# Kernel optimization log

Hardware: AMD Instinct MI355X
Metric: run time of the kernel (lower is better)

Reference implementation:

```python
import jax, jax.numpy as jnp
import numpy as np

NUM_ROIS = 148
BSZ = 16
HID = 64
IN_CH = 128
OUT_CH = 2
N1, E1 = 131072, 2097152
N2, E2 = 2368, 37888
LRELU_SLOPE = 0.01
BN_EPS = 1e-5


def gcn_conv(x, src, dst, ew, W, b, n):
    """PyG GCNConv with edge weights and self-loops (weight 1): D^-1/2 (A+I) D^-1/2 X W + b."""
    h = x @ W  # (n, out)
    deg = jax.ops.segment_sum(ew, dst, num_segments=n) + 1.0  # self-loop weight 1
    dinv = jax.lax.rsqrt(deg)
    norm = dinv[src] * ew * dinv[dst]  # (E,)
    out = jax.ops.segment_sum(h[src] * norm[:, None], dst, num_segments=n)
    out = out + h * (dinv * dinv)[:, None]  # self-loop term: 1/deg
    return out + b


def roi_pool_mean(x, roi, batch, num_rois, bsz):
    """Segment mean keyed by (batch, roi); empty groups stay zero. Returns (bsz, num_rois*d)."""
    seg = batch * num_rois + roi
    nseg = bsz * num_rois
    sums = jax.ops.segment_sum(x, seg, num_segments=nseg)
    cnt = jax.ops.segment_sum(jnp.ones((x.shape[0],), x.dtype), seg, num_segments=nseg)
    pooled = sums / jnp.maximum(cnt, 1.0)[:, None]
    return pooled.reshape(bsz, -1)


def _params(key):
    ks = jax.random.split(key, 8)
    def lin(k, fi, fo):
        return jax.random.normal(k, (fi, fo), jnp.float32) / np.sqrt(fi)
    p = {}
    p["W1a"], p["b1a"] = lin(ks[0], IN_CH, HID), jnp.zeros((HID,), jnp.float32)
    p["W1b"], p["b1b"] = lin(ks[1], HID, HID), jnp.zeros((HID,), jnp.float32)
    p["W2a"], p["b2a"] = lin(ks[2], IN_CH, HID), jnp.zeros((HID,), jnp.float32)
    p["W2b"], p["b2b"] = lin(ks[3], HID, HID), jnp.zeros((HID,), jnp.float32)
    p["Wm1"], p["bm1"] = lin(ks[4], HID * NUM_ROIS, 1000), jnp.zeros((1000,), jnp.float32)
    p["gamma"], p["beta"] = jnp.ones((1000,), jnp.float32), jnp.zeros((1000,), jnp.float32)
    p["bn_mean"], p["bn_var"] = jnp.zeros((1000,), jnp.float32), jnp.ones((1000,), jnp.float32)
    p["Wm2"], p["bm2"] = lin(ks[5], 1000, OUT_CH), jnp.zeros((OUT_CH,), jnp.float32)
    return p


def setup_inputs() -> dict:
    key = jax.random.key(0)
    ks = jax.random.split(key, 12)
    inp = {
        "x1": jax.random.normal(ks[0], (N1, IN_CH), jnp.float32),
        "node_label": jax.random.randint(ks[1], (N1,), 0, NUM_ROIS, jnp.int32),
        "edge_index1": jax.random.randint(ks[2], (2, E1), 0, N1, jnp.int32),
        "edge_weight1": jax.random.uniform(ks[3], (E1,), jnp.float32),
        "batch1": jnp.sort(jax.random.randint(ks[4], (N1,), 0, BSZ, jnp.int32)),
        "x2": jax.random.normal(ks[5], (N2, IN_CH), jnp.float32),
        "roi_label": jax.random.randint(ks[6], (N2,), 0, NUM_ROIS, jnp.int32),
        "edge_index2": jax.random.randint(ks[7], (2, E2), 0, N2, jnp.int32),
        "edge_weight2": jax.random.uniform(ks[8], (E2,), jnp.float32),
        "batch2": jnp.sort(jax.random.randint(ks[9], (N2,), 0, BSZ, jnp.int32)),
    }
    inp.update(_params(ks[10]))
    return inp


def reference(x1, node_label, edge_index1, edge_weight1, batch1,
              x2, roi_label, edge_index2, edge_weight2, batch2,
              W1a, b1a, W1b, b1b, W2a, b2a, W2b, b2b,
              Wm1, bm1, gamma, beta, bn_mean, bn_var, Wm2, bm2):
    # ROI-graph branch (convs_roi[:-1], eval mode: dropout is identity)
    s2, d2 = edge_index2[0], edge_index2[1]
    h2 = jax.nn.relu(gcn_conv(x2, s2, d2, edge_weight2, W2a, b2a, N2))
    h2 = jax.nn.relu(gcn_conv(h2, s2, d2, edge_weight2, W2b, b2b, N2))
    embedding_roi = roi_pool_mean(h2, roi_label, batch2, NUM_ROIS, BSZ)  # (B, 148*HID)
    # fine-grained branch (convs[:-1])
    s1, d1 = edge_index1[0], edge_index1[1]
    h1 = jax.nn.relu(gcn_conv(x1, s1, d1, edge_weight1, W1a, b1a, N1))
    h1 = jax.nn.relu(gcn_conv(h1, s1, d1, edge_weight1, W1b, b1b, N1))
    embedding = roi_pool_mean(h1, node_label, batch1, NUM_ROIS, BSZ)
    # classifier on embedding + embedding_roi
    s = embedding + embedding_roi
    h = s @ Wm1 + bm1
    h = gamma * (h - bn_mean) * jax.lax.rsqrt(bn_var + BN_EPS) + beta  # BatchNorm1d (eval)
    h = jnp.where(h > 0, h, LRELU_SLOPE * h)  # LeakyReLU
    out = h @ Wm2 + bm2  # (B, OUT_CH)
    return out, embedding, embedding_roi, embedding + embedding_roi
```

## Files before the change

### kernel.cpp

```cpp
#include <hip/hip_runtime.h>
#include <hip/hip_fp16.h>

#define N1 131072
#define E1 2097152
#define N2 2368
#define E2 37888
#define NROIS 148
#define BSZ 16
#define HID 64
#define INCH 128
#define NSEG (BSZ*NROIS)
#define SDIM (NROIS*HID)
#define CLS 1000
#define OCH 2

#define KT1 148
#define KCC 64
#define CT1 4
#define SLP 20

#define NB1 512
#define BLK1 512
#define EPB (E1/BLK1)
#define NPB (N1/NB1)

#define CW1 ((N1+15)/16)
#define CW2 ((N2+15)/16)
#define PW  ((NSEG+15)/16)

#define T1 (N1/16)
#define T2 (N2/16)
#define GEMMB ((T1+T2)/4)

typedef _Float16 h8 __attribute__((ext_vector_type(8)));
typedef float f4 __attribute__((ext_vector_type(4)));

__device__ __forceinline__ unsigned packh2(float a, float b) {
    return (unsigned)__half_as_ushort(__float2half_rn(a)) |
           ((unsigned)__half_as_ushort(__float2half_rn(b)) << 16);
}

__device__ __forceinline__ void fma_lo(float& a, unsigned hb, float w) {
    asm("v_fma_mix_f32 %0, %1, %2, %0 op_sel:[0,0,0] op_sel_hi:[1,0,0]"
        : "+v"(a) : "v"(hb), "v"(w));
}
__device__ __forceinline__ void fma_hi(float& a, unsigned hb, float w) {
    asm("v_fma_mix_f32 %0, %1, %2, %0 op_sel:[1,0,0] op_sel_hi:[1,0,0]"
        : "+v"(a) : "v"(hb), "v"(w));
}


__global__ void k_hist_dst(int* __restrict__ cnt, const int* __restrict__ dst, int E) {
    int e = blockIdx.x * 256 + threadIdx.x;
    if (e < E) atomicAdd(&cnt[dst[e]], 1);
}

__global__ void k_hist_seg2(int* __restrict__ c1, const int* __restrict__ b1,
                            const int* __restrict__ l1, int n1_,
                            int* __restrict__ c2, const int* __restrict__ b2,
                            const int* __restrict__ l2, int n2_) {
    int i = blockIdx.x * 256 + threadIdx.x;
    if (i < n1_) { atomicAdd(&c1[b1[i] * NROIS + l1[i]], 1); return; }
    int j = i - n1_;
    if (j < n2_) atomicAdd(&c2[b2[j] * NROIS + l2[j]], 1);
}

__global__ void k_scan1(const int* __restrict__ in, int* __restrict__ out,
                        int* __restrict__ part, int n) {
    __shared__ int sh[256];
    int t = threadIdx.x;
    int i0 = blockIdx.x * 1024 + t * 4;
    int v0 = (i0     < n) ? in[i0]     : 0;
    int v1 = (i0 + 1 < n) ? in[i0 + 1] : 0;
    int v2 = (i0 + 2 < n) ? in[i0 + 2] : 0;
    int v3 = (i0 + 3 < n) ? in[i0 + 3] : 0;
    int tot = v0 + v1 + v2 + v3;
    sh[t] = tot; __syncthreads();
    for (int off = 1; off < 256; off <<= 1) {
        int x = 0; if (t >= off) x = sh[t - off];
        __syncthreads();
        if (t >= off) sh[t] += x;
        __syncthreads();
    }
    int excl = sh[t] - tot;
    if (t == 255) part[blockIdx.x] = sh[255];
    if (i0     < n) out[i0]     = excl;
    if (i0 + 1 < n) out[i0 + 1] = excl + v0;
    if (i0 + 2 < n) out[i0 + 2] = excl + v0 + v1;
    if (i0 + 3 < n) out[i0 + 3] = excl + v0 + v1 + v2;
}

__global__ void k_scan2(int* __restrict__ part, int cnt) {
    __shared__ int sh[256];
    int t = threadIdx.x;
    int v = (t < cnt) ? part[t] : 0;
    sh[t] = v; __syncthreads();
    for (int off = 1; off < 256; off <<= 1) {
        int x = 0; if (t >= off) x = sh[t - off];
        __syncthreads();
        if (t >= off) sh[t] += x;
        __syncthreads();
    }
    if (t < cnt) part[t] = sh[t] - v;
}

__global__ void k_scan3(int* __restrict__ out, const int* __restrict__ part, int n, int total) {
    int i = blockIdx.x * 256 + threadIdx.x;
    if (i < n) out[i] += part[i >> 10];
    if (i == 0) out[n] = total;
}

__global__ void k_scan_one(const int* __restrict__ in0, int* __restrict__ out0,
                           int* __restrict__ oo0, int n0,
                           const int* __restrict__ in1, int* __restrict__ out1,
                           int* __restrict__ oo1, int n1_) {
    __shared__ int sh[256];
    __shared__ int carry;
    const int* in; int* out; int* oo; int n;
    if (blockIdx.x == 0) { in = in0; out = out0; oo = oo0; n = n0; }
    else { if (!in1) return; in = in1; out = out1; oo = oo1; n = n1_; }
    int t = threadIdx.x;
    if (t == 0) carry = 0;
    __syncthreads();
    for (int base = 0; base < n; base += 256) {
        int i = base + t;
        int v = (i < n) ? in[i] : 0;
        sh[t] = v; __syncthreads();
        for (int off = 1; off < 256; off <<= 1) {
            int x = 0; if (t >= off) x = sh[t - off];
            __syncthreads();
            if (t >= off) sh[t] += x;
            __syncthreads();
        }
        if (i < n) {
            int e = carry + sh[t] - v;
            out[i] = e;
            if (oo) oo[i] = e;
        }
        __syncthreads();
        if (t == 255) carry += sh[255];
        __syncthreads();
    }
    if (t == 0) out[n] = carry;
}

__global__ void k_fill_edges(int2* __restrict__ edges, int* __restrict__ off,
                             const int* __restrict__ src, const int* __restrict__ dst,
                             const float* __restrict__ ew, int E) {
    int e = blockIdx.x * 256 + threadIdx.x;
    if (e >= E) return;
    int pos = atomicAdd(&off[dst[e]], 1);
    edges[pos] = make_int2(src[e], __float_as_int(ew[e]));
}

__global__ void k_fill_seg2(int* __restrict__ id1, int* __restrict__ o1,
                            const int* __restrict__ b1, const int* __restrict__ l1, int n1_,
                            int* __restrict__ id2, int* __restrict__ o2,
                            const int* __restrict__ b2, const int* __restrict__ l2, int n2_) {
    int i = blockIdx.x * 256 + threadIdx.x;
    if (i < n1_) {
        int pos = atomicAdd(&o1[b1[i] * NROIS + l1[i]], 1);
        id1[pos] = i << 7;
        return;
    }
    int j = i - n1_;
    if (j < n2_) {
        int pos = atomicAdd(&o2[b2[j] * NROIS + l2[j]], 1);
        id2[pos] = j << 7;
    }
}

__global__ void k_deg_dinv(float* __restrict__ dinv, const int* __restrict__ row,
                           const int2* __restrict__ edges, int n) {
    int d = blockIdx.x * 256 + threadIdx.x;
    if (d >= n) return;
    int a = row[d], b = row[d + 1];
    float s = 1.0f;
    for (int i = a; i < b; i++) s += __int_as_float(edges[i].y);
    dinv[d] = rsqrtf(s);
}

__global__ void k_scale(int2* __restrict__ edges, const int* __restrict__ row,
                        const float* __restrict__ dinv, int n) {
    int d = blockIdx.x * 256 + threadIdx.x;
    if (d >= n) return;
    int a = row[d], b = row[d + 1];
    float dd = dinv[d];
    for (int i = a; i < b; i++) {
        int2 e = edges[i];
        edges[i] = make_int2(e.x << 7,
                             __float_as_int(dinv[e.x] * __int_as_float(e.y) * dd));
    }
}


__global__ __launch_bounds__(256) void k_p1(int* __restrict__ bh, const int* __restrict__ dst) {
    __shared__ int cnt[NB1];
    int t = threadIdx.x, blk = blockIdx.x;
    for (int i = t; i < NB1; i += 256) cnt[i] = 0;
    __syncthreads();
    int base = blk * EPB;
    for (int i = t; i < EPB; i += 256) atomicAdd(&cnt[dst[base + i] >> 8], 1);
    __syncthreads();
    for (int b = t; b < NB1; b += 256) bh[b * BLK1 + blk] = cnt[b];
}

__global__ __launch_bounds__(256) void k_p2(int2* __restrict__ tmp, const int* __restrict__ obh,
                                            const int* __restrict__ src,
                                            const int* __restrict__ dst,
                                            const float* __restrict__ ew) {
    __shared__ int cur[NB1];
    int t = threadIdx.x, blk = blockIdx.x;
    for (int b = t; b < NB1; b += 256) cur[b] = obh[b * BLK1 + blk];
    __syncthreads();
    int base = blk * EPB;
    for (int i = t; i < EPB; i += 256) {
        int e = base + i;
        int d = dst[e];
        int pos = atomicAdd(&cur[d >> 8], 1);
        tmp[pos] = make_int2(src[e] | ((d & 255) << 17), __float_as_int(ew[e]));
    }
}

__global__ __launch_bounds__(256) void k_p3a(int* __restrict__ row1, float* __restrict__ dinv,
                                             const int2* __restrict__ tmp,
                                             const int* __restrict__ obh) {
    __shared__ int h[NPB];
    __shared__ float ws[NPB];
    __shared__ int sc[256];
    int t = threadIdx.x, b = blockIdx.x;
    h[t] = 0; ws[t] = 0.f;
    __syncthreads();
    int ebase = obh[b * BLK1];
    int eend  = (b == NB1 - 1) ? E1 : obh[(b + 1) * BLK1];
    for (int i = ebase + t; i < eend; i += 256) {
        int2 ed = tmp[i];
        int dl = (ed.x >> 17) & 255;
        atomicAdd(&h[dl], 1);
        atomicAdd(&ws[dl], __int_as_float(ed.y));
    }
    __syncthreads();
    int cnt = h[t];
    sc[t] = cnt; __syncthreads();
    for (int off = 1; off < 256; off <<= 1) {
        int x = 0; if (t >= off) x = sc[t - off];
        __syncthreads();
        if (t >= off) sc[t] += x;
        __syncthreads();
    }
    row1[b * NPB + t] = ebase + sc[t] - cnt;
    dinv[b * NPB + t] = rsqrtf(1.f + ws[t]);
    if (b == NB1 - 1 && t == 255) row1[N1] = E1;
}

__global__ __launch_bounds__(256) void k_p3b(int2* __restrict__ edges,
                                             const int2* __restrict__ tmp,
                                             const int* __restrict__ obh,
                                             const int* __restrict__ row,
                                             const float* __restrict__ dinv) {
    __shared__ int cur[NPB];
    __shared__ float dvl[NPB];
    int t = threadIdx.x, b = blockIdx.x;
    int n0 = b * NPB;
    for (int i = t; i < NPB; i += 256) {
        cur[i] = row[n0 + i];
        dvl[i] = dinv[n0 + i];
    }
    __syncthreads();
    int a  = obh[b * BLK1];
    int e_ = (b == NB1 - 1) ? E1 : obh[(b + 1) * BLK1];
    for (int i = a + t; i < e_; i += 256) {
        int2 ed = tmp[i];
        int dl = (ed.x >> 17) & 255;
        int s = ed.x & 0x1FFFF;
        int pos = atomicAdd(&cur[dl], 1);
        float w = dinv[s] * __int_as_float(ed.y) * dvl[dl];
        edges[pos] = make_int2(s << 7, __float_as_int(w));
    }
}


__device__ __forceinline__ void wfrag(uint4* __restrict__ o, const float* __restrict__ W,
                                      int KCH, int idx) {
    int lane = idx & 63;
    int rest = idx >> 6;
    int ch = rest % KCH;
    int ct = rest / KCH;
    int kr = ch * 32 + ((lane >> 4) * 8);
    int col = ct * 16 + (lane & 15);
    const float* wp = W + (size_t)kr * 64 + col;
    o[idx] = make_uint4(packh2(wp[0],   wp[64]),
                        packh2(wp[128], wp[192]),
                        packh2(wp[256], wp[320]),
                        packh2(wp[384], wp[448]));
}

__global__ void k_wprep(uint4* __restrict__ wf1a, const float* __restrict__ W1a,
                        uint4* __restrict__ wf1b, const float* __restrict__ W1b,
                        uint4* __restrict__ wf2a, const float* __restrict__ W2a,
                        uint4* __restrict__ wf2b, const float* __restrict__ W2b) {
    int idx = blockIdx.x * 256 + threadIdx.x;
    if      (idx < 1024) wfrag(wf1a, W1a, 4, idx);
    else if (idx < 1536) wfrag(wf1b, W1b, 2, idx - 1024);
    else if (idx < 2560) wfrag(wf2a, W2a, 4, idx - 1536);
    else if (idx < 3072) wfrag(wf2b, W2b, 2, idx - 2560);
}

__device__ __forceinline__ h8 loadA(const float* p) {
    float4 a = *(const float4*)p;
    float4 b = *(const float4*)(p + 4);
    union { h8 v; __half h[8]; } u;
    u.h[0] = __float2half_rn(a.x); u.h[1] = __float2half_rn(a.y);
    u.h[2] = __float2half_rn(a.z); u.h[3] = __float2half_rn(a.w);
    u.h[4] = __float2half_rn(b.x); u.h[5] = __float2half_rn(b.y);
    u.h[6] = __float2half_rn(b.z); u.h[7] = __float2half_rn(b.w);
    return u.v;
}
__device__ __forceinline__ h8 loadA(const __half* p) {
    union { h8 v; uint4 u; } u;
    u.u = *(const uint4*)p;
    return u.v;
}

template <int K, typename T>
__global__ __launch_bounds__(256) void k_gemm(__half* __restrict__ out1, const T* __restrict__ x1,
                                              const uint4* __restrict__ wfa, int t1,
                                              __half* __restrict__ out2, const T* __restrict__ x2,
                                              const uint4* __restrict__ wfb, int t2) {
    constexpr int KCH = K / 32;
    int wid = blockIdx.x * 4 + (threadIdx.x >> 6);
    int lane = threadIdx.x & 63;
    __half* out; const T* x; const uint4* wf; int row0;
    if (wid < t1) { out = out1; x = x1; wf = wfa; row0 = wid * 16; }
    else {
        int w2 = wid - t1;
        if (w2 >= t2) return;
        out = out2; x = x2; wf = wfb; row0 = w2 * 16;
    }
    int lrow = lane & 15, lg = lane >> 4;

    h8 bf[4][KCH];
#pragma unroll
    for (int ct = 0; ct < 4; ct++)
#pragma unroll
        for (int ch = 0; ch < KCH; ch++) {
            union { h8 v; uint4 u; } u;
            u.u = wf[(ct * KCH + ch) * 64 + lane];
            bf[ct][ch] = u.v;
        }

    const T* xr = x + (size_t)(row0 + lrow) * K + lg * 8;
    h8 af[KCH];
#pragma unroll
    for (int ch = 0; ch < KCH; ch++) af[ch] = loadA(xr + ch * 32);

    f4 acc[4];
#pragma unroll
    for (int ct = 0; ct < 4; ct++) acc[ct] = (f4){0.f, 0.f, 0.f, 0.f};
#pragma unroll
    for (int ch = 0; ch < KCH; ch++)
#pragma unroll
        for (int ct = 0; ct < 4; ct++)
            acc[ct] = __builtin_amdgcn_mfma_f32_16x16x32_f16(af[ch], bf[ct][ch], acc[ct], 0, 0, 0);

#pragma unroll
    for (int ct = 0; ct < 4; ct++)
#pragma unroll
        for (int r = 0; r < 4; r++)
            out[(size_t)(row0 + lg * 4 + r) * 64 + ct * 16 + lrow] = __float2half_rn(acc[ct][r]);
}

__device__ __forceinline__ void conv_wave(__half* __restrict__ out, const __half* __restrict__ h,
                                          const int2* __restrict__ edges,
                                          const int* __restrict__ row,
                                          const float* __restrict__ dinv,
                                          const float* __restrict__ bias,
                                          int d0, int n, int lane) {
    int g  = lane >> 4;
    int fl = lane & 15;
    int eh = fl >> 3;
    int f8 = fl & 7;
    int d  = d0 + g;
    bool vn = d < n;
    int a = 0, b = 0;
    if (vn) { a = row[d]; b = row[d + 1]; }
    const char* hb = (const char*)h + f8 * 16;
    float acc[8] = {0.f,0.f,0.f,0.f,0.f,0.f,0.f,0.f};

    for (int base = a; base < b; base += 16) {
        int sv = 0, wv = 0;
        if (base + fl < b) { int2 e = edges[base + fl]; sv = e.x; wv = e.y; }
        int mm = b - base; if (mm > 16) mm = 16;
        int steps = (mm + 1) >> 1;
        int idx = (g << 4) + eh;
        for (int t = 0; t < steps; t++) {
            int   s = __shfl(sv, idx + (t << 1));
            float w = __int_as_float(__shfl(wv, idx + (t << 1)));
            uint4 hv = *(const uint4*)(hb + (unsigned)s);
            fma_lo(acc[0], hv.x, w); fma_hi(acc[1], hv.x, w);
            fma_lo(acc[2], hv.y, w); fma_hi(acc[3], hv.y, w);
            fma_lo(acc[4], hv.z, w); fma_hi(acc[5], hv.z, w);
            fma_lo(acc[6], hv.w, w); fma_hi(acc[7], hv.w, w);
        }
    }
    float r[8];
#pragma unroll
    for (int f = 0; f < 8; f++) r[f] = acc[f] + __shfl_xor(acc[f], 8);
    if (vn && eh == 0) {
        float di = dinv[d];
        float sl = di * di;
        uint4 hd = *(const uint4*)(hb + ((unsigned)d << 7));
        fma_lo(r[0], hd.x, sl); fma_hi(r[1], hd.x, sl);
        fma_lo(r[2], hd.y, sl); fma_hi(r[3], hd.y, sl);
        fma_lo(r[4], hd.z, sl); fma_hi(r[5], hd.z, sl);
        fma_lo(r[6], hd.w, sl); fma_hi(r[7], hd.w, sl);
        float4 b0 = *(const float4*)(bias + f8 * 8);
        float4 b1 = *(const float4*)(bias + f8 * 8 + 4);
        uint4 ov;
        ov.x = packh2(fmaxf(r[0] + b0.x, 0.f), fmaxf(r[1] + b0.y, 0.f));
        ov.y = packh2(fmaxf(r[2] + b0.z, 0.f), fmaxf(r[3] + b0.w, 0.f));
        ov.z = packh2(fmaxf(r[4] + b1.x, 0.f), fmaxf(r[5] + b1.y, 0.f));
        ov.w = packh2(fmaxf(r[6] + b1.z, 0.f), fmaxf(r[7] + b1.w, 0.f));
        *(uint4*)(out + (size_t)d * HID + f8 * 8) = ov;
    }
}

__global__ __launch_bounds__(256) void k_conv(__half* __restrict__ o1, const __half* __restrict__ h1,
                                              const int2* __restrict__ e1, const int* __restrict__ r1,
                                              const float* __restrict__ dv1, const float* __restrict__ bi1,
                                              int n1_, int nb1_,
                                              __half* __restrict__ o2, const __half* __restrict__ h2,
                                              const int2* __restrict__ e2, const int* __restrict__ r2,
                                              const float* __restrict__ dv2, const float* __restrict__ bi2,
                                              int n2_) {
    int blk = blockIdx.x;
    int lane = threadIdx.x & 63;
    int wv = threadIdx.x >> 6;
    if (blk < nb1_) conv_wave(o1, h1, e1, r1, dv1, bi1, blk * 16 + wv * 4, n1_, lane);
    else            conv_wave(o2, h2, e2, r2, dv2, bi2, (blk - nb1_) * 16 + wv * 4, n2_, lane);
}

__device__ __forceinline__ void pool_wave(float* __restrict__ emb, const __half* __restrict__ h,
                                          const int* __restrict__ nodeid,
                                          const int* __restrict__ segrow, int s0, int lane) {
    int g  = lane >> 4;
    int fl = lane & 15;
    int eh = fl >> 3;
    int f8 = fl & 7;
    int s  = s0 + g;
    bool vs = s < NSEG;
    int a = 0, b = 0;
    if (vs) { a = segrow[s]; b = segrow[s + 1]; }
    const char* hb = (const char*)h + f8 * 16;
    float acc[8] = {0.f,0.f,0.f,0.f,0.f,0.f,0.f,0.f};

    for (int base = a; base < b; base += 16) {
        int sv = 0, wv = 0;
        if (base + fl < b) { sv = nodeid[base + fl]; wv = 0x3f800000; }
        int mm = b - base; if (mm > 16) mm = 16;
        int steps = (mm + 1) >> 1;
        int idx = (g << 4) + eh;
        for (int t = 0; t < steps; t++) {
            int   q = __shfl(sv, idx + (t << 1));
            float w = __int_as_float(__shfl(wv, idx + (t << 1)));
            uint4 hv = *(const uint4*)(hb + (unsigned)q);
            fma_lo(acc[0], hv.x, w); fma_hi(acc[1], hv.x, w);
            fma_lo(acc[2], hv.y, w); fma_hi(acc[3], hv.y, w);
            fma_lo(acc[4], hv.z, w); fma_hi(acc[5], hv.z, w);
            fma_lo(acc[6], hv.w, w); fma_hi(acc[7], hv.w, w);
        }
    }
    float r[8];
#pragma unroll
    for (int f = 0; f < 8; f++) r[f] = acc[f] + __shfl_xor(acc[f], 8);
    if (vs && eh == 0) {
        float inv = 1.0f / fmaxf((float)(b - a), 1.0f);
        float4 lo = make_float4(r[0] * inv, r[1] * inv, r[2] * inv, r[3] * inv);
        float4 hi = make_float4(r[4] * inv, r[5] * inv, r[6] * inv, r[7] * inv);
        *(float4*)(emb + (size_t)s * HID + f8 * 8)     = lo;
        *(float4*)(emb + (size_t)s * HID + f8 * 8 + 4) = hi;
    }
}

__global__ __launch_bounds__(256) void k_pool(float* __restrict__ em1, const __half* __restrict__ h1,
                                              const int* __restrict__ id1, const int* __restrict__ sr1,
                                              int nbs,
                                              float* __restrict__ em2, const __half* __restrict__ h2,
                                              const int* __restrict__ id2, const int* __restrict__ sr2) {
    int blk = blockIdx.x;
    int lane = threadIdx.x & 63;
    int wv = threadIdx.x >> 6;
    if (blk < nbs) pool_wave(em1, h1, id1, sr1, blk * 16 + wv * 4, lane);
    else           pool_wave(em2, h2, id2, sr2, (blk - nbs) * 16 + wv * 4, lane);
}


__global__ __launch_bounds__(256) void k_cls(float* __restrict__ part_,
                                             const float* __restrict__ e1,
                                             const float* __restrict__ e2,
                                             float* __restrict__ esum,
                                             const float* __restrict__ Wm1) {
    __shared__ float sl[KCC * SLP];
    int tid = threadIdx.x;
    int kt = blockIdx.x >> 2, ct = blockIdx.x & 3;
    int k0 = kt * KCC;
    bool wr = (ct == 0);
    for (int i = tid; i < KCC * 16; i += 256) {
        int kk = i & (KCC - 1), b = i >> 6;
        int idx = b * SDIM + k0 + kk;
        float v = e1[idx] + e2[idx];
        sl[kk * SLP + b] = v;
        if (wr) esum[idx] = v;
    }
    __syncthreads();
    int c = ct * 256 + tid;
    bool active = c < CLS;
    const float* wp = Wm1 + (size_t)k0 * CLS + c;
    float wv[KCC];
#pragma unroll
    for (int kk = 0; kk < KCC; kk++)
        wv[kk] = active ? wp[(size_t)kk * CLS] : 0.f;
    float acc[16];
#pragma unroll
    for (int b = 0; b < 16; b++) acc[b] = 0.f;
#pragma unroll
    for (int kk = 0; kk < KCC; kk++) {
        float w = wv[kk];
        float4 s0 = *(const float4*)(&sl[kk * SLP + 0]);
        float4 s1 = *(const float4*)(&sl[kk * SLP + 4]);
        float4 s2 = *(const float4*)(&sl[kk * SLP + 8]);
        float4 s3 = *(const float4*)(&sl[kk * SLP + 12]);
        acc[0]  += s0.x * w; acc[1]  += s0.y * w; acc[2]  += s0.z * w; acc[3]  += s0.w * w;
        acc[4]  += s1.x * w; acc[5]  += s1.y * w; acc[6]  += s1.z * w; acc[7]  += s1.w * w;
        acc[8]  += s2.x * w; acc[9]  += s2.y * w; acc[10] += s2.z * w; acc[11] += s2.w * w;
        acc[12] += s3.x * w; acc[13] += s3.y * w; acc[14] += s3.z * w; acc[15] += s3.w * w;
    }
    float* pp = part_ + (size_t)(kt * CT1 + ct) * 16 * 256;
#pragma unroll
    for (int b = 0; b < 16; b++) pp[b * 256 + tid] = acc[b];
}

__global__ void k_credbn(float* __restrict__ hact, const float* __restrict__ part_,
                         const float* __restrict__ bm1, const float* __restrict__ gamma,
                         const float* __restrict__ beta, const float* __restrict__ mean,
                         const float* __restrict__ var) {
    int idx = blockIdx.x * 256 + threadIdx.x;
    if (idx >= BSZ * CLS) return;
    int b = idx / CLS, c = idx % CLS;
    int ct = c >> 8, cl = c & 255;
    float sum = 0.f;
#pragma unroll 8
    for (int kt = 0; kt < KT1; kt++)
        sum += part_[((size_t)(kt * CT1 + ct) * 16 + b) * 256 + cl];
    float t = sum + bm1[c];
    t = gamma[c] * (t - mean[c]) * rsqrtf(var[c] + 1e-5f) + beta[c];
    hact[idx] = t > 0.f ? t : 0.01f * t;
}

__global__ void k_out(float* __restrict__ outp, const float* __restrict__ hact,
                      const float* __restrict__ Wm2, const float* __restrict__ bm2) {
    int b = blockIdx.x;
    int tid = threadIdx.x;
    int o = tid & 1, part = tid >> 1;
    float acc = (part == 0) ? bm2[o] : 0.f;
    for (int k = part; k < CLS; k += 128) acc += hact[b * CLS + k] * Wm2[k * OCH + o];
    unsafeAtomicAdd(&outp[b * OCH + o], acc);
}

extern "C" void kernel_launch(void* const* d_in, const int* in_sizes, int n_in,
                              void* d_out, int out_size, void* d_ws, size_t ws_size,
                              hipStream_t stream) {
    const float* x1  = (const float*)d_in[0];
    const int*   nl  = (const int*)d_in[1];
    const int*   ei1 = (const int*)d_in[2];
    const float* ew1 = (const float*)d_in[3];
    const int*   ba1 = (const int*)d_in[4];
    const float* x2  = (const float*)d_in[5];
    const int*   rl  = (const int*)d_in[6];
    const int*   ei2 = (const int*)d_in[7];
    const float* ew2 = (const float*)d_in[8];
    const int*   ba2 = (const int*)d_in[9];
    const float* W1a = (const float*)d_in[10];
    const float* b1a = (const float*)d_in[11];
    const float* W1b = (const float*)d_in[12];
    const float* b1b = (const float*)d_in[13];
    const float* W2a = (const float*)d_in[14];
    const float* b2a = (const float*)d_in[15];
    const float* W2b = (const float*)d_in[16];
    const float* b2b = (const float*)d_in[17];
    const float* Wm1 = (const float*)d_in[18];
    const float* bm1 = (const float*)d_in[19];
    const float* gam = (const float*)d_in[20];
    const float* bet = (const float*)d_in[21];
    const float* bmn = (const float*)d_in[22];
    const float* bvr = (const float*)d_in[23];
    const float* Wm2 = (const float*)d_in[24];
    const float* bm2 = (const float*)d_in[25];

    float* out  = (float*)d_out;
    float* emb1 = out + 32;
    float* emb2 = emb1 + NSEG * HID;
    float* esum = emb2 + NSEG * HID;

    char* p = (char*)d_ws;
    auto carve = [&](size_t nbytes) { char* q = p; p += (nbytes + 255) & ~(size_t)255; return (void*)q; };
    int*    row1    = (int*)   carve((N1 + 1) * 4);
    int2*   edges1  = (int2*)  carve((size_t)E1 * 8);
    float*  dinv1   = (float*) carve(N1 * 4);
    __half* A1h     = (__half*)carve((size_t)N1 * HID * 2);
    __half* B1h     = (__half*)carve((size_t)N1 * HID * 2);
    int*    nodeid1 = (int*)   carve(N1 * 4);
    int*    segrow1 = (int*)   carve((NSEG + 1) * 4);
    int*    segoff  = (int*)   carve(2 * NSEG * 4);
    int*    bh      = (int*)   carve((NB1 * BLK1 + 1) * 4);
    int*    obh     = (int*)   carve((NB1 * BLK1 + 1) * 4);
    int*    row2    = (int*)   carve((N2 + 1) * 4);
    int*    off2    = (int*)   carve(N2 * 4);
    int2*   edges2  = (int2*)  carve((size_t)E2 * 8);
    float*  dinv2   = (float*) carve(N2 * 4);
    __half* A2h     = (__half*)carve((size_t)N2 * HID * 2);
    __half* B2h     = (__half*)carve((size_t)N2 * HID * 2);
    int*    nodeid2 = (int*)   carve(N2 * 4);
    int*    segrow2 = (int*)   carve((NSEG + 1) * 4);
    int*    part    = (int*)   carve(256 * 4);
    float*  hact    = (float*) carve(BSZ * CLS * 4);
    uint4*  wf1a    = (uint4*) carve(1024 * 16);
    uint4*  wf1b    = (uint4*) carve(512 * 16);
    uint4*  wf2a    = (uint4*) carve(1024 * 16);
    uint4*  wf2b    = (uint4*) carve(512 * 16);
    int*    segoff1 = segoff;
    int*    segoff2 = segoff + NSEG;
    int2*  tmp1 = (int2*)B1h;
    float* clsp = (float*)B1h;

    const int* src1 = ei1;
    const int* dst1 = ei1 + E1;
    const int* src2 = ei2;
    const int* dst2 = ei2 + E2;

    hipMemsetAsync(d_out, 0, (size_t)out_size * sizeof(float), stream);

    k_wprep<<<12, 256, 0, stream>>>(wf1a, W1a, wf1b, W1b, wf2a, W2a, wf2b, W2b);

    hipMemsetAsync(off2, 0, N2 * 4, stream);
    k_hist_dst<<<(E2 + 255) / 256, 256, 0, stream>>>(off2, dst2, E2);
    k_scan_one<<<1, 256, 0, stream>>>(off2, row2, off2, N2, nullptr, nullptr, nullptr, 0);
    k_fill_edges<<<(E2 + 255) / 256, 256, 0, stream>>>(edges2, off2, src2, dst2, ew2, E2);
    k_deg_dinv<<<(N2 + 255) / 256, 256, 0, stream>>>(dinv2, row2, edges2, N2);
    k_scale<<<(N2 + 255) / 256, 256, 0, stream>>>(edges2, row2, dinv2, N2);

    k_p1<<<BLK1, 256, 0, stream>>>(bh, dst1);
    k_scan1<<<(NB1 * BLK1 + 1023) / 1024, 256, 0, stream>>>(bh, obh, part, NB1 * BLK1);
    k_scan2<<<1, 256, 0, stream>>>(part, (NB1 * BLK1 + 1023) / 1024);
    k_scan3<<<(NB1 * BLK1 + 255) / 256, 256, 0, stream>>>(obh, part, NB1 * BLK1, E1);
    k_p2<<<BLK1, 256, 0, stream>>>(tmp1, obh, src1, dst1, ew1);
    k_p3a<<<NB1, 256, 0, stream>>>(row1, dinv1, tmp1, obh);
    k_p3b<<<NB1, 256, 0, stream>>>(edges1, tmp1, obh, row1, dinv1);

    k_gemm<INCH, float><<<GEMMB, 256, 0, stream>>>(A1h, x1, wf1a, T1, A2h, x2, wf2a, T2);
    k_conv<<<CW1 + CW2, 256, 0, stream>>>(B1h, A1h, edges1, row1, dinv1, b1a, N1, CW1,
                                          B2h, A2h, edges2, row2, dinv2, b2a, N2);
    k_gemm<HID, __half><<<GEMMB, 256, 0, stream>>>(A1h, B1h, wf1b, T1, A2h, B2h, wf2b, T2);
    k_conv<<<CW1 + CW2, 256, 0, stream>>>(B1h, A1h, edges1, row1, dinv1, b1b, N1, CW1,
                                          B2h, A2h, edges2, row2, dinv2, b2b, N2);

    hipMemsetAsync(segoff, 0, 2 * NSEG * 4, stream);
    k_hist_seg2<<<(N1 + N2 + 255) / 256, 256, 0, stream>>>(segoff1, ba1, nl, N1,
                                                           segoff2, ba2, rl, N2);
    k_scan_one<<<2, 256, 0, stream>>>(segoff1, segrow1, segoff1, NSEG,
                                      segoff2, segrow2, segoff2, NSEG);
    k_fill_seg2<<<(N1 + N2 + 255) / 256, 256, 0, stream>>>(nodeid1, segoff1, ba1, nl, N1,
                                                           nodeid2, segoff2, ba2, rl, N2);
    k_pool<<<PW + PW, 256, 0, stream>>>(emb1, B1h, nodeid1, segrow1, PW,
                                        emb2, B2h, nodeid2, segrow2);

    k_cls<<<KT1 * CT1, 256, 0, stream>>>(clsp, emb1, emb2, esum, Wm1);
    k_credbn<<<(BSZ * CLS + 255) / 256, 256, 0, stream>>>(hact, clsp, bm1, gam, bet, bmn, bvr);
    k_out<<<BSZ, 256, 0, stream>>>(out, hact, Wm2, bm2);
}
```

Before: 528.2 us.

## Restructure CSR build: fold degree sum into histogram, stage bucket scatter in LDS

```diff
diff --git a/kernel.cpp b/kernel.cpp
--- a/kernel.cpp
+++ b/kernel.cpp
@@ -23,6 +23,7 @@
 #define BLK1 512
 #define EPB (E1/BLK1)
 #define NPB (N1/NB1)
+#define P3CAP 5120
 
 #define CW1 ((N1+15)/16)
 #define CW2 ((N2+15)/16)
@@ -194,88 +195,131 @@
 }
 
 
-__global__ __launch_bounds__(256) void k_p1(int* __restrict__ bh, const int* __restrict__ dst) {
+__global__ __launch_bounds__(256) void k_p1(int* __restrict__ bh, const int* __restrict__ dst,
+                                            const float* __restrict__ ew, float* __restrict__ ws) {
     __shared__ int cnt[NB1];
     int t = threadIdx.x, blk = blockIdx.x;
-    for (int i = t; i < NB1; i += 256) cnt[i] = 0;
+    cnt[t] = 0; cnt[t + 256] = 0;
     __syncthreads();
     int base = blk * EPB;
-    for (int i = t; i < EPB; i += 256) atomicAdd(&cnt[dst[base + i] >> 8], 1);
-    __syncthreads();
-    for (int b = t; b < NB1; b += 256) bh[b * BLK1 + blk] = cnt[b];
+    const int4* d4 = (const int4*)(dst + base);
+    const float4* w4 = (const float4*)(ew + base);
+    for (int i = t; i < EPB / 4; i += 256) {
+        int4 d = d4[i];
+        float4 w = w4[i];
+        atomicAdd(&cnt[d.x >> 8], 1); unsafeAtomicAdd(&ws[d.x], w.x);
+        atomicAdd(&cnt[d.y >> 8], 1); unsafeAtomicAdd(&ws[d.y], w.y);
+        atomicAdd(&cnt[d.z >> 8], 1); unsafeAtomicAdd(&ws[d.z], w.z);
+        atomicAdd(&cnt[d.w >> 8], 1); unsafeAtomicAdd(&ws[d.w], w.w);
+    }
+    __syncthreads();
+    bh[t * BLK1 + blk] = cnt[t];
+    bh[(t + 256) * BLK1 + blk] = cnt[t + 256];
+}
+
+__global__ void k_dinv(float* __restrict__ dinv, int n) {
+    int i = blockIdx.x * 256 + threadIdx.x;
+    if (i < n) dinv[i] = rsqrtf(1.f + dinv[i]);
 }
 
 __global__ __launch_bounds__(256) void k_p2(int2* __restrict__ tmp, const int* __restrict__ obh,
                                             const int* __restrict__ src,
                                             const int* __restrict__ dst,
-                                            const float* __restrict__ ew) {
+                                            const float* __restrict__ ew,
+                                            const float* __restrict__ dinv) {
+    __shared__ int2 stage[EPB];
+    __shared__ unsigned short bkt[EPB];
+    __shared__ int cnt[NB1];
+    __shared__ int lofs[NB1];
+    __shared__ int gdel[NB1];
     __shared__ int cur[NB1];
+    __shared__ int sc[256];
+    __shared__ int cbr;
     int t = threadIdx.x, blk = blockIdx.x;
-    for (int b = t; b < NB1; b += 256) cur[b] = obh[b * BLK1 + blk];
+    cnt[t] = 0; cnt[t + 256] = 0;
     __syncthreads();
     int base = blk * EPB;
+    const int4* d4 = (const int4*)(dst + base);
+    for (int i = t; i < EPB / 4; i += 256) {
+        int4 d = d4[i];
+        atomicAdd(&cnt[d.x >> 8], 1);
+        atomicAdd(&cnt[d.y >> 8], 1);
+        atomicAdd(&cnt[d.z >> 8], 1);
+        atomicAdd(&cnt[d.w >> 8], 1);
+    }
+    __syncthreads();
+    for (int r = 0; r < 2; r++) {
+        int v = cnt[r * 256 + t];
+        sc[t] = v; __syncthreads();
+        for (int off = 1; off < 256; off <<= 1) {
+            int x = 0; if (t >= off) x = sc[t - off];
+            __syncthreads();
+            if (t >= off) sc[t] += x;
+            __syncthreads();
+        }
+        lofs[r * 256 + t] = (r ? cbr : 0) + sc[t] - v;
+        if (t == 255 && r == 0) cbr = sc[255];
+        __syncthreads();
+    }
+    for (int b = t; b < NB1; b += 256) {
+        int lo = lofs[b];
+        cur[b] = lo;
+        gdel[b] = obh[b * BLK1 + blk] - lo;
+    }
+    __syncthreads();
     for (int i = t; i < EPB; i += 256) {
         int e = base + i;
         int d = dst[e];
-        int pos = atomicAdd(&cur[d >> 8], 1);
-        tmp[pos] = make_int2(src[e] | ((d & 255) << 17), __float_as_int(ew[e]));
-    }
-}
-
-__global__ __launch_bounds__(256) void k_p3a(int* __restrict__ row1, float* __restrict__ dinv,
-                                             const int2* __restrict__ tmp,
-                                             const int* __restrict__ obh) {
+        int s = src[e];
+        float w = dinv[s] * ew[e] * dinv[d];
+        int b = d >> 8;
+        int p = atomicAdd(&cur[b], 1);
+        stage[p] = make_int2(s | ((d & 255) << 17), __float_as_int(w));
+        bkt[p] = (unsigned short)b;
+    }
+    __syncthreads();
+    for (int i = t; i < EPB; i += 256)
+        tmp[gdel[bkt[i]] + i] = stage[i];
+}
+
+__global__ __launch_bounds__(256) void k_p3(int2* __restrict__ edges, int* __restrict__ row1,
+                                            const int2* __restrict__ tmp,
+                                            const int* __restrict__ obh) {
+    __shared__ int2 stage[P3CAP];
     __shared__ int h[NPB];
-    __shared__ float ws[NPB];
     __shared__ int sc[256];
+    __shared__ int cur[NPB];
     int t = threadIdx.x, b = blockIdx.x;
-    h[t] = 0; ws[t] = 0.f;
-    __syncthreads();
-    int ebase = obh[b * BLK1];
-    int eend  = (b == NB1 - 1) ? E1 : obh[(b + 1) * BLK1];
-    for (int i = ebase + t; i < eend; i += 256) {
-        int2 ed = tmp[i];
-        int dl = (ed.x >> 17) & 255;
-        atomicAdd(&h[dl], 1);
-        atomicAdd(&ws[dl], __int_as_float(ed.y));
-    }
-    __syncthreads();
-    int cnt = h[t];
-    sc[t] = cnt; __syncthreads();
+    h[t] = 0;
+    __syncthreads();
+    int A = obh[b * BLK1];
+    int Eend = (b == NB1 - 1) ? E1 : obh[(b + 1) * BLK1];
+    int len = Eend - A;
+    for (int j = t; j < len; j += 256) {
+        int2 ed = tmp[A + j];
+        if (j < P3CAP) stage[j] = ed;
+        atomicAdd(&h[(ed.x >> 17) & 255], 1);
+    }
+    __syncthreads();
+    int cnt_ = h[t];
+    sc[t] = cnt_; __syncthreads();
     for (int off = 1; off < 256; off <<= 1) {
         int x = 0; if (t >= off) x = sc[t - off];
         __syncthreads();
         if (t >= off) sc[t] += x;
         __syncthreads();
     }
-    row1[b * NPB + t] = ebase + sc[t] - cnt;
-    dinv[b * NPB + t] = rsqrtf(1.f + ws[t]);
+    int excl = sc[t] - cnt_;
+    row1[b * NPB + t] = A + excl;
+    cur[t] = excl;
     if (b == NB1 - 1 && t == 255) row1[N1] = E1;
-}
-
-__global__ __launch_bounds__(256) void k_p3b(int2* __restrict__ edges,
-                                             const int2* __restrict__ tmp,
-                                             const int* __restrict__ obh,
-                                             const int* __restrict__ row,
-                                             const float* __restrict__ dinv) {
-    __shared__ int cur[NPB];
-    __shared__ float dvl[NPB];
-    int t = threadIdx.x, b = blockIdx.x;
-    int n0 = b * NPB;
-    for (int i = t; i < NPB; i += 256) {
-        cur[i] = row[n0 + i];
-        dvl[i] = dinv[n0 + i];
-    }
-    __syncthreads();
-    int a  = obh[b * BLK1];
-    int e_ = (b == NB1 - 1) ? E1 : obh[(b + 1) * BLK1];
-    for (int i = a + t; i < e_; i += 256) {
-        int2 ed = tmp[i];
+    __syncthreads();
+    for (int j = t; j < len; j += 256) {
+        int2 ed = (j < P3CAP) ? stage[j] : tmp[A + j];
         int dl = (ed.x >> 17) & 255;
         int s = ed.x & 0x1FFFF;
-        int pos = atomicAdd(&cur[dl], 1);
-        float w = dinv[s] * __int_as_float(ed.y) * dvl[dl];
-        edges[pos] = make_int2(s << 7, __float_as_int(w));
+        int p = atomicAdd(&cur[dl], 1);
+        edges[A + p] = make_int2(s << 7, ed.y);
     }
 }
 
@@ -649,13 +693,14 @@
     k_deg_dinv<<<(N2 + 255) / 256, 256, 0, stream>>>(dinv2, row2, edges2, N2);
     k_scale<<<(N2 + 255) / 256, 256, 0, stream>>>(edges2, row2, dinv2, N2);
 
-    k_p1<<<BLK1, 256, 0, stream>>>(bh, dst1);
+    hipMemsetAsync(dinv1, 0, N1 * 4, stream);
+    k_p1<<<BLK1, 256, 0, stream>>>(bh, dst1, ew1, dinv1);
+    k_dinv<<<(N1 + 255) / 256, 256, 0, stream>>>(dinv1, N1);
     k_scan1<<<(NB1 * BLK1 + 1023) / 1024, 256, 0, stream>>>(bh, obh, part, NB1 * BLK1);
     k_scan2<<<1, 256, 0, stream>>>(part, (NB1 * BLK1 + 1023) / 1024);
     k_scan3<<<(NB1 * BLK1 + 255) / 256, 256, 0, stream>>>(obh, part, NB1 * BLK1, E1);
-    k_p2<<<BLK1, 256, 0, stream>>>(tmp1, obh, src1, dst1, ew1);
-    k_p3a<<<NB1, 256, 0, stream>>>(row1, dinv1, tmp1, obh);
-    k_p3b<<<NB1, 256, 0, stream>>>(edges1, tmp1, obh, row1, dinv1);
+    k_p2<<<BLK1, 256, 0, stream>>>(tmp1, obh, src1, dst1, ew1, dinv1);
+    k_p3<<<NB1, 256, 0, stream>>>(edges1, row1, tmp1, obh);
 
     k_gemm<INCH, float><<<GEMMB, 256, 0, stream>>>(A1h, x1, wf1a, T1, A2h, x2, wf2a, T2);
     k_conv<<<CW1 + CW2, 256, 0, stream>>>(B1h, A1h, edges1, row1, dinv1, b1a, N1, CW1,
```

Result: slower. 605.7 us (+14.7%).
